# Kernel optimization log

Measured on AMD Instinct MI355X. Metric: run time of the kernel, lower is better.

Reference implementation:

```python
import jax, jax.numpy as jnp
import numpy as np
from jax import lax

STATE_LEN = 5
N_BASE = 4
C = N_BASE ** STATE_LEN          # 1024 CRF states
NZ = N_BASE + 1                  # 5 incoming transitions per state
FEAT = 320
KW = 19
STRIDE = 5
SCALE = 5.0


def _transition_idx():
    # bonito CTC_CRF.idx: predecessor state for each (state, transition) pair
    a = np.arange(C)
    idx = np.concatenate([a[:, None], np.repeat(a, N_BASE).reshape(N_BASE, -1).T], axis=1)
    return jnp.asarray(idx, dtype=jnp.int32)  # [C, NZ]


def setup_inputs() -> dict:
    key = jax.random.key(0)
    ks = jax.random.split(key, 5)
    x = jax.random.normal(ks[0], (32, 1, 4000), jnp.float32)
    conv_w = jax.random.normal(ks[1], (FEAT, 1, KW), jnp.float32) * 0.1
    conv_b = jax.random.normal(ks[2], (FEAT,), jnp.float32) * 0.1
    lin_w = jax.random.normal(ks[3], (FEAT, C * NZ), jnp.float32) * (1.0 / np.sqrt(FEAT))
    lin_b = jax.random.normal(ks[4], (C * NZ,), jnp.float32) * 0.1
    return {"x": x, "conv_w": conv_w, "conv_b": conv_b, "lin_w": lin_w, "lin_b": lin_b}


def _encoder(x, conv_w, conv_b, lin_w, lin_b):
    # x: [N, 1, L] -> strided conv -> [N, FEAT, T]
    y = lax.conv_general_dilated(x, conv_w, (STRIDE,), "SAME",
                                 dimension_numbers=("NCH", "OIH", "NCH"))
    y = jnp.tanh(y + conv_b[None, :, None])
    y = jnp.transpose(y, (2, 0, 1))  # [T, N, FEAT]
    # scaled-tanh CRF output head -> [T, N, C*NZ]
    return SCALE * jnp.tanh(jnp.einsum("tnf,fc->tnc", y, lin_w) + lin_b)


def _logZ(scores, idx):
    # log-semiring forward algorithm (alpha_0 = beta_T = 0)
    T, N, _ = scores.shape
    Ms = scores.reshape(T, N, C, NZ)
    alpha0 = jnp.zeros((N, C), scores.dtype)

    def step(alpha, Ms_t):  # Ms_t: [N, C, NZ], alpha: [N, C]
        return jax.nn.logsumexp(Ms_t + alpha[:, idx], axis=2), None

    alpha, _ = lax.scan(step, alpha0, Ms)
    return jax.nn.logsumexp(alpha, axis=1)  # [N]


def reference(x, conv_w, conv_b, lin_w, lin_b):
    idx = _transition_idx()
    scores = _encoder(x, conv_w, conv_b, lin_w, lin_b).astype(jnp.float32)  # [T, N, 5120]
    T = scores.shape[0]
    # GlobalNorm: scores - logZ / T, broadcast over time and channel dims
    return scores - _logZ(scores, idx)[:, None] / T
```

## Files before the change

kernel.cpp:

```cpp
#include <hip/hip_runtime.h>
#include <hip/hip_bf16.h>
#include <hip/hip_fp16.h>
#include <type_traits>


typedef __attribute__((ext_vector_type(8))) short bf16x8;
typedef __attribute__((ext_vector_type(4))) float f32x4;

#define T_STEPS 800
#define NBATCH 32
#define FEAT 320
#define CNZ 5120
#define MROWS (T_STEPS * NBATCH)
#define FSPLIT 480
#define BSTEPS (T_STEPS - FSPLIT)

__device__ __forceinline__ float fast_tanh(float x) {
    float e = exp2f(x * 2.8853900817779268f);
    return 1.0f - 2.0f * __builtin_amdgcn_rcpf(e + 1.0f);
}

__global__ __launch_bounds__(320) void conv_kernel(
    const float* __restrict__ x, const float* __restrict__ w,
    const float* __restrict__ b, __hip_bfloat16* __restrict__ y) {
    int m = blockIdx.x;
    int t = m >> 5, n = m & 31;
    int f = threadIdx.x;
    __shared__ float xs[19];
    int base = t * 5 - 7;
    if (f < 19) {
        int pos = base + f;
        xs[f] = (pos >= 0 && pos < 4000) ? x[n * 4000 + pos] : 0.0f;
    }
    __syncthreads();
    float acc = b[f];
#pragma unroll
    for (int k = 0; k < 19; ++k) acc = fmaf(xs[k], w[f * 19 + k], acc);
    y[(size_t)m * FEAT + f] = __float2bfloat16(fast_tanh(acc));
}

__global__ __launch_bounds__(256) void transpose_w(
    const float* __restrict__ W, __hip_bfloat16* __restrict__ Wt) {
    __shared__ float tile[64][65];
    int nb = blockIdx.x * 64, kb = blockIdx.y * 64;
    int tx = threadIdx.x & 63, ty = threadIdx.x >> 6;
#pragma unroll
    for (int r = 0; r < 64; r += 4)
        tile[ty + r][tx] = W[(size_t)(kb + ty + r) * CNZ + nb + tx];
    __syncthreads();
#pragma unroll
    for (int r = 0; r < 64; r += 4) {
        int nn = ty + r;
        Wt[(size_t)(nb + nn) * FEAT + kb + tx] = __float2bfloat16(tile[tx][nn]);
    }
}

#define GBM 128
#define GBN 128
#define GBK 64
#define LDK 72

__global__ __launch_bounds__(256) void gemm_kernel(
    const __hip_bfloat16* __restrict__ A,
    const __hip_bfloat16* __restrict__ Bt,
    const float* __restrict__ bias,
    float* __restrict__ out,
    __half* __restrict__ s16) {
    __shared__ __align__(16) short As[GBM * LDK];
    __shared__ __align__(16) short Bs[GBN * LDK];
    const int K = FEAT;
    int bm0 = blockIdx.x * GBM;
    int bn0 = blockIdx.y * GBN;
    int tid = threadIdx.x;
    int wave = tid >> 6, lane = tid & 63;
    int wm = (wave >> 1) * 64, wn = (wave & 1) * 64;
    int col = lane & 15, quad = lane >> 4;

    f32x4 acc[4][4];
#pragma unroll
    for (int i = 0; i < 4; ++i)
#pragma unroll
        for (int j = 0; j < 4; ++j) acc[i][j] = (f32x4){0.f, 0.f, 0.f, 0.f};

    for (int k0 = 0; k0 < K; k0 += GBK) {
#pragma unroll
        for (int p = 0; p < 4; ++p) {
            int i = p * 256 + tid;
            int row = i >> 3, cg = i & 7;
            *(int4*)&As[row * LDK + cg * 8] =
                *(const int4*)&A[(size_t)(bm0 + row) * K + k0 + cg * 8];
            *(int4*)&Bs[row * LDK + cg * 8] =
                *(const int4*)&Bt[(size_t)(bn0 + row) * K + k0 + cg * 8];
        }
        __syncthreads();
#pragma unroll
        for (int kk = 0; kk < GBK; kk += 32) {
            bf16x8 af[4], bfr[4];
#pragma unroll
            for (int i = 0; i < 4; ++i)
                af[i] = *(bf16x8*)&As[(wm + i * 16 + col) * LDK + kk + quad * 8];
#pragma unroll
            for (int j = 0; j < 4; ++j)
                bfr[j] = *(bf16x8*)&Bs[(wn + j * 16 + col) * LDK + kk + quad * 8];
#pragma unroll
            for (int i = 0; i < 4; ++i)
#pragma unroll
                for (int j = 0; j < 4; ++j)
                    acc[i][j] = __builtin_amdgcn_mfma_f32_16x16x32_bf16(
                        af[i], bfr[j], acc[i][j], 0, 0, 0);
        }
        __syncthreads();
    }
#pragma unroll
    for (int j = 0; j < 4; ++j) {
        int n_g = bn0 + wn + j * 16 + col;
        float bj = bias[n_g];
#pragma unroll
        for (int i = 0; i < 4; ++i) {
            int m_base = bm0 + wm + i * 16 + quad * 4;
#pragma unroll
            for (int r = 0; r < 4; ++r) {
                size_t idx = (size_t)(m_base + r) * CNZ + n_g;
                float v = 5.0f * fast_tanh(acc[i][j][r] + bj);
                out[idx] = v;
                if (s16) s16[idx] = __float2half(v);
            }
        }
    }
}


__device__ __forceinline__ float lse5_2(float s0, float s1, float s2, float s3,
                                        float s4, float a0, float a1, float a2,
                                        float a3, float a4) {
    const float L2E = 1.4426950408889634f;
    float x0 = fmaf(s0, L2E, a0);
    float x1 = fmaf(s1, L2E, a1);
    float x2 = fmaf(s2, L2E, a2);
    float x3 = fmaf(s3, L2E, a3);
    float x4 = fmaf(s4, L2E, a4);
    float mx = fmaxf(fmaxf(fmaxf(x0, x1), fmaxf(x2, x3)), x4);
    float sum = __builtin_amdgcn_exp2f(x0 - mx) + __builtin_amdgcn_exp2f(x1 - mx) +
                __builtin_amdgcn_exp2f(x2 - mx) + __builtin_amdgcn_exp2f(x3 - mx) +
                __builtin_amdgcn_exp2f(x4 - mx);
    return __builtin_amdgcn_logf(sum) + mx;
}

__device__ __forceinline__ float cvh(ushort u) { __half h = *(__half*)&u; return __half2float(h); }
__device__ __forceinline__ float cvh(float f) { return f; }

template<bool FP16>
__global__ __launch_bounds__(512) void fb_kernel(
    const void* __restrict__ sc, float* __restrict__ alphaF,
    float* __restrict__ betaB) {
    __shared__ __align__(16) float A0[1024];
    __shared__ __align__(16) float A1[1024];
    const int tid = threadIdx.x;
    const int n = blockIdx.x & 31;
    const int dir = blockIdx.x >> 5;

    *(float2*)&A0[2 * tid] = make_float2(0.f, 0.f);
    __syncthreads();

    const size_t row = (size_t)NBATCH * CNZ;

    if (dir == 0) {
        const int q = tid >> 1;
        const uint* fbu = (const uint*)((const __half*)sc + (size_t)n * CNZ) +
                          (size_t)tid * 5;
        const float2* fbf = (const float2*)((const float*)sc + (size_t)n * CNZ +
                          (size_t)tid * 10);

#define LDF(P, TT) do { int tc_ = (TT) < FSPLIT ? (TT) : (FSPLIT - 1);         \
    if constexpr (FP16) { const uint* pp_ = fbu + (size_t)tc_ * 81920;         \
        P[0] = pp_[0]; P[1] = pp_[1]; P[2] = pp_[2]; P[3] = pp_[3]; P[4] = pp_[4]; } \
    else { const float2* pp_ = fbf + (size_t)tc_ * 81920; float2* d_ = (float2*)P; \
        d_[0] = pp_[0]; d_[1] = pp_[1]; d_[2] = pp_[2]; d_[3] = pp_[3]; d_[4] = pp_[4]; } \
} while (0)

#define UNP(P, s) do { if constexpr (FP16) {                                   \
        float2 f0_ = __half22float2(*(__half2*)&P[0]);                         \
        float2 f1_ = __half22float2(*(__half2*)&P[1]);                         \
        float2 f2_ = __half22float2(*(__half2*)&P[2]);                         \
        float2 f3_ = __half22float2(*(__half2*)&P[3]);                         \
        float2 f4_ = __half22float2(*(__half2*)&P[4]);                         \
        s[0]=f0_.x; s[1]=f0_.y; s[2]=f1_.x; s[3]=f1_.y; s[4]=f2_.x;            \
        s[5]=f2_.y; s[6]=f3_.x; s[7]=f3_.y; s[8]=f4_.x; s[9]=f4_.y; }          \
    else { const float* f_ = (const float*)P;                                  \
        s[0]=f_[0]; s[1]=f_[1]; s[2]=f_[2]; s[3]=f_[3]; s[4]=f_[4];            \
        s[5]=f_[5]; s[6]=f_[6]; s[7]=f_[7]; s[8]=f_[8]; s[9]=f_[9]; }          \
} while (0)

#define FSTEP(P, TT, cur, nxt) do { float s_[10]; UNP(P, s_); LDF(P, TT);      \
    float aq0_ = (cur)[q], aq1_ = (cur)[q + 256];                              \
    float aq2_ = (cur)[q + 512], aq3_ = (cur)[q + 768];                        \
    float2 ao_ = *(const float2*)&(cur)[2 * tid];                              \
    float r0_ = lse5_2(s_[0], s_[1], s_[2], s_[3], s_[4], ao_.x, aq0_, aq1_, aq2_, aq3_); \
    float r1_ = lse5_2(s_[5], s_[6], s_[7], s_[8], s_[9], ao_.y, aq0_, aq1_, aq2_, aq3_); \
    *(float2*)&(nxt)[2 * tid] = make_float2(r0_, r1_);                         \
    __syncthreads();                                                           \
} while (0)

        uint P0[10], P1[10], P2[10], P3[10];
        LDF(P0, 0); LDF(P1, 1); LDF(P2, 2); LDF(P3, 3);
        for (int t = 0; t < FSPLIT; t += 4) {
            FSTEP(P0, t + 4, A0, A1);
            FSTEP(P1, t + 5, A1, A0);
            FSTEP(P2, t + 6, A0, A1);
            FSTEP(P3, t + 7, A1, A0);
        }
        *(float2*)&alphaF[(size_t)n * 1024 + 2 * tid] = *(const float2*)&A0[2 * tid];
    } else {
        using ET = std::conditional_t<FP16, ushort, float>;
        const int p0 = 2 * tid;
        const int g = p0 & 255;
        const int hi = p0 >> 8;
        const size_t o_self = (size_t)10 * tid;
        const size_t gb = (size_t)20 * g + 1 + hi;
        const ET* bb = (const ET*)sc + (size_t)n * CNZ;
        const int sbase = (8 * tid) & 1023;

#define LDB(E, KK) do { int kc_ = (KK) < BSTEPS ? (KK) : (BSTEPS - 1);         \
    const ET* pb_ = bb + (size_t)(T_STEPS - 1 - kc_) * row;                    \
    E[0] = pb_[o_self];      E[1] = pb_[gb];       E[2] = pb_[gb + 5];         \
    E[3] = pb_[gb + 10];     E[4] = pb_[gb + 15];  E[5] = pb_[o_self + 5];     \
    E[6] = pb_[gb + 20];     E[7] = pb_[gb + 25];  E[8] = pb_[gb + 30];        \
    E[9] = pb_[gb + 35];                                                       \
} while (0)

#define BSTEP(E, KK, cur, nxt) do { float s_[10];                              \
    s_[0]=cvh(E[0]); s_[1]=cvh(E[1]); s_[2]=cvh(E[2]); s_[3]=cvh(E[3]);        \
    s_[4]=cvh(E[4]); s_[5]=cvh(E[5]); s_[6]=cvh(E[6]); s_[7]=cvh(E[7]);        \
    s_[8]=cvh(E[8]); s_[9]=cvh(E[9]); LDB(E, KK);                              \
    float2 bs_ = *(const float2*)&(cur)[2 * tid];                              \
    float4 b0_ = *(const float4*)&(cur)[sbase];                                \
    float4 b1_ = *(const float4*)&(cur)[sbase + 4];                            \
    float r0_ = lse5_2(s_[0], s_[1], s_[2], s_[3], s_[4], bs_.x, b0_.x, b0_.y, b0_.z, b0_.w); \
    float r1_ = lse5_2(s_[5], s_[6], s_[7], s_[8], s_[9], bs_.y, b1_.x, b1_.y, b1_.z, b1_.w); \
    *(float2*)&(nxt)[2 * tid] = make_float2(r0_, r1_);                         \
    __syncthreads();                                                           \
} while (0)

        ET E0[10], E1[10], E2[10], E3[10];
        LDB(E0, 0); LDB(E1, 1); LDB(E2, 2); LDB(E3, 3);
        for (int k = 0; k < BSTEPS; k += 4) {
            BSTEP(E0, k + 4, A0, A1);
            BSTEP(E1, k + 5, A1, A0);
            BSTEP(E2, k + 6, A0, A1);
            BSTEP(E3, k + 7, A1, A0);
        }
        *(float2*)&betaB[(size_t)n * 1024 + 2 * tid] = *(const float2*)&A0[2 * tid];
    }
}

__global__ __launch_bounds__(256) void combine_kernel(
    const float* __restrict__ aF, const float* __restrict__ bB,
    float* __restrict__ corr) {
    __shared__ float R[256];
    int n = blockIdx.x, tid = threadIdx.x;
    float4 a = *(const float4*)&aF[(size_t)n * 1024 + 4 * tid];
    float4 b = *(const float4*)&bB[(size_t)n * 1024 + 4 * tid];
    float x0 = a.x + b.x, x1 = a.y + b.y, x2 = a.z + b.z, x3 = a.w + b.w;
    float m = fmaxf(fmaxf(x0, x1), fmaxf(x2, x3));
    R[tid] = m;
    __syncthreads();
#pragma unroll
    for (int s = 128; s > 0; s >>= 1) {
        if (tid < s) R[tid] = fmaxf(R[tid], R[tid + s]);
        __syncthreads();
    }
    float mx = R[0];
    __syncthreads();
    float sm = exp2f(x0 - mx) + exp2f(x1 - mx) + exp2f(x2 - mx) + exp2f(x3 - mx);
    R[tid] = sm;
    __syncthreads();
#pragma unroll
    for (int s = 128; s > 0; s >>= 1) {
        if (tid < s) R[tid] += R[tid + s];
        __syncthreads();
    }
    if (tid == 0)
        corr[n] = (log2f(R[0]) + mx) * 0.6931471805599453f * (1.0f / (float)T_STEPS);
}

__global__ __launch_bounds__(256) void sub_kernel(
    float* __restrict__ out, const float* __restrict__ corr) {
    size_t i4 = (size_t)blockIdx.x * blockDim.x + threadIdx.x;
    float cc = corr[(i4 / (CNZ / 4)) & (NBATCH - 1)];
    float4* o4 = (float4*)out;
    float4 v = o4[i4];
    v.x -= cc; v.y -= cc; v.z -= cc; v.w -= cc;
    o4[i4] = v;
}

extern "C" void kernel_launch(void* const* d_in, const int* in_sizes, int n_in,
                              void* d_out, int out_size, void* d_ws, size_t ws_size,
                              hipStream_t stream) {
    const float* x      = (const float*)d_in[0];
    const float* conv_w = (const float*)d_in[1];
    const float* conv_b = (const float*)d_in[2];
    const float* lin_w  = (const float*)d_in[3];
    const float* lin_b  = (const float*)d_in[4];
    float* out = (float*)d_out;

    const size_t Y_OFF    = 0;
    const size_t WT_OFF   = 16384000;
    const size_t CORR_OFF = 19660800;
    const size_t AF_OFF   = 19661056;
    const size_t BB_OFF   = 19792128;
    const size_t S16_OFF  = 19923200;
    const size_t NEED16   = S16_OFF + (size_t)MROWS * CNZ * 2;

    char* ws = (char*)d_ws;
    __hip_bfloat16* y  = (__hip_bfloat16*)(ws + Y_OFF);
    __hip_bfloat16* wt = (__hip_bfloat16*)(ws + WT_OFF);
    float* corr = (float*)(ws + CORR_OFF);
    float* aF   = (float*)(ws + AF_OFF);
    float* bB   = (float*)(ws + BB_OFF);
    bool fp16_path = ws_size >= NEED16;
    __half* s16 = fp16_path ? (__half*)(ws + S16_OFF) : nullptr;

    conv_kernel<<<MROWS, 320, 0, stream>>>(x, conv_w, conv_b, y);
    transpose_w<<<dim3(CNZ / 64, FEAT / 64), 256, 0, stream>>>(lin_w, wt);
    gemm_kernel<<<dim3(MROWS / GBM, CNZ / GBN), 256, 0, stream>>>(y, wt, lin_b, out, s16);
    if (fp16_path)
        fb_kernel<true><<<64, 512, 0, stream>>>(s16, aF, bB);
    else
        fb_kernel<false><<<64, 512, 0, stream>>>(out, aF, bB);
    combine_kernel<<<NBATCH, 256, 0, stream>>>(aF, bB, corr);
    sub_kernel<<<(out_size / 4) / 256, 256, 0, stream>>>(out, corr);
}
```

Baseline: 1.416 ms.

## Add transposed fp16 score copy for backward pass and rebuild output from fp16

The GEMM epilogue now also writes a second fp16 copy of the scores, laid out transposed per transition so the backward recursion can issue wide contiguous loads instead of scattered scalar gathers. Because backward steps should now cost about the same as forward steps, the forward/backward split point moves to the midpoint. When workspace allows, the GEMM skips the fp32 output write and the final subtraction kernel rebuilds the fp32 output from the fp16 scores. This cuts global memory traffic but gives outputs with only fp16 precision, and it needs twice the fp16 workspace.

```diff
diff --git a/kernel.cpp b/kernel.cpp
--- a/kernel.cpp
+++ b/kernel.cpp
@@ -1,23 +1,29 @@
 #include <hip/hip_runtime.h>
 #include <hip/hip_bf16.h>
 #include <hip/hip_fp16.h>
-#include <type_traits>
 
 
 typedef __attribute__((ext_vector_type(8))) short bf16x8;
 typedef __attribute__((ext_vector_type(4))) float f32x4;
+typedef unsigned int uint4u __attribute__((ext_vector_type(4), aligned(4)));
 
 #define T_STEPS 800
 #define NBATCH 32
 #define FEAT 320
 #define CNZ 5120
 #define MROWS (T_STEPS * NBATCH)
-#define FSPLIT 480
+#define FSPLIT 400
 #define BSTEPS (T_STEPS - FSPLIT)
+#define ROWB 327680
 
 __device__ __forceinline__ float fast_tanh(float x) {
     float e = exp2f(x * 2.8853900817779268f);
     return 1.0f - 2.0f * __builtin_amdgcn_rcpf(e + 1.0f);
+}
+
+__device__ __forceinline__ float2 h2f(uint u) {
+    __half2 h = *(__half2*)&u;
+    return __half22float2(h);
 }
 
 __global__ __launch_bounds__(320) void conv_kernel(
@@ -65,7 +71,9 @@
     const __hip_bfloat16* __restrict__ Bt,
     const float* __restrict__ bias,
     float* __restrict__ out,
-    __half* __restrict__ s16) {
+    __half* __restrict__ s16n,
+    __half* __restrict__ s16t,
+    int write_out) {
     __shared__ __align__(16) short As[GBM * LDK];
     __shared__ __align__(16) short Bs[GBN * LDK];
     const int K = FEAT;
@@ -115,15 +123,21 @@
     for (int j = 0; j < 4; ++j) {
         int n_g = bn0 + wn + j * 16 + col;
         float bj = bias[n_g];
+        uint c = (uint)n_g / 5u;
+        uint z = (uint)n_g - 5u * c;
+        size_t t_off = (size_t)z * 1024 + c;
 #pragma unroll
         for (int i = 0; i < 4; ++i) {
             int m_base = bm0 + wm + i * 16 + quad * 4;
 #pragma unroll
             for (int r = 0; r < 4; ++r) {
-                size_t idx = (size_t)(m_base + r) * CNZ + n_g;
+                int m = m_base + r;
+                size_t idx = (size_t)m * CNZ + n_g;
                 float v = 5.0f * fast_tanh(acc[i][j][r] + bj);
-                out[idx] = v;
-                if (s16) s16[idx] = __float2half(v);
+                if (write_out) out[idx] = v;
+                __half hv = __float2half(v);
+                if (s16n) s16n[idx] = hv;
+                if (s16t) s16t[(size_t)m * CNZ + t_off] = hv;
             }
         }
     }
@@ -146,13 +160,10 @@
     return __builtin_amdgcn_logf(sum) + mx;
 }
 
-__device__ __forceinline__ float cvh(ushort u) { __half h = *(__half*)&u; return __half2float(h); }
-__device__ __forceinline__ float cvh(float f) { return f; }
-
-template<bool FP16>
+template<int MODE>
 __global__ __launch_bounds__(512) void fb_kernel(
-    const void* __restrict__ sc, float* __restrict__ alphaF,
-    float* __restrict__ betaB) {
+    const void* __restrict__ nat, const void* __restrict__ tr,
+    float* __restrict__ alphaF, float* __restrict__ betaB) {
     __shared__ __align__(16) float A0[1024];
     __shared__ __align__(16) float A1[1024];
     const int tid = threadIdx.x;
@@ -162,92 +173,148 @@
     *(float2*)&A0[2 * tid] = make_float2(0.f, 0.f);
     __syncthreads();
 
-    const size_t row = (size_t)NBATCH * CNZ;
-
     if (dir == 0) {
         const int q = tid >> 1;
-        const uint* fbu = (const uint*)((const __half*)sc + (size_t)n * CNZ) +
-                          (size_t)tid * 5;
-        const float2* fbf = (const float2*)((const float*)sc + (size_t)n * CNZ +
-                          (size_t)tid * 10);
-
-#define LDF(P, TT) do { int tc_ = (TT) < FSPLIT ? (TT) : (FSPLIT - 1);         \
-    if constexpr (FP16) { const uint* pp_ = fbu + (size_t)tc_ * 81920;         \
-        P[0] = pp_[0]; P[1] = pp_[1]; P[2] = pp_[2]; P[3] = pp_[3]; P[4] = pp_[4]; } \
-    else { const float2* pp_ = fbf + (size_t)tc_ * 81920; float2* d_ = (float2*)P; \
-        d_[0] = pp_[0]; d_[1] = pp_[1]; d_[2] = pp_[2]; d_[3] = pp_[3]; d_[4] = pp_[4]; } \
-} while (0)
-
-#define UNP(P, s) do { if constexpr (FP16) {                                   \
-        float2 f0_ = __half22float2(*(__half2*)&P[0]);                         \
-        float2 f1_ = __half22float2(*(__half2*)&P[1]);                         \
-        float2 f2_ = __half22float2(*(__half2*)&P[2]);                         \
-        float2 f3_ = __half22float2(*(__half2*)&P[3]);                         \
-        float2 f4_ = __half22float2(*(__half2*)&P[4]);                         \
-        s[0]=f0_.x; s[1]=f0_.y; s[2]=f1_.x; s[3]=f1_.y; s[4]=f2_.x;            \
-        s[5]=f2_.y; s[6]=f3_.x; s[7]=f3_.y; s[8]=f4_.x; s[9]=f4_.y; }          \
-    else { const float* f_ = (const float*)P;                                  \
-        s[0]=f_[0]; s[1]=f_[1]; s[2]=f_[2]; s[3]=f_[3]; s[4]=f_[4];            \
-        s[5]=f_[5]; s[6]=f_[6]; s[7]=f_[7]; s[8]=f_[8]; s[9]=f_[9]; }          \
-} while (0)
-
-#define FSTEP(P, TT, cur, nxt) do { float s_[10]; UNP(P, s_); LDF(P, TT);      \
+
+        if constexpr (MODE == 2) {
+            const char* fbn = (const char*)nat +
+                              ((size_t)n * CNZ + (size_t)tid * 10) * 2;
+
+#define LDF2(V, S, TT) do { int tc_ = (TT) < FSPLIT ? (TT) : (FSPLIT - 1);     \
+    const char* p_ = fbn + (size_t)tc_ * ROWB;                                 \
+    V = *(const uint4u*)p_; S = *(const uint*)(p_ + 16);                       \
+} while (0)
+
+#define FSTEP2(V, S, TT, cur, nxt) do {                                        \
+    float2 f0_ = h2f(V.x), f1_ = h2f(V.y), f2_ = h2f(V.z), f3_ = h2f(V.w);     \
+    float2 f4_ = h2f(S);                                                       \
+    LDF2(V, S, TT);                                                            \
     float aq0_ = (cur)[q], aq1_ = (cur)[q + 256];                              \
     float aq2_ = (cur)[q + 512], aq3_ = (cur)[q + 768];                        \
     float2 ao_ = *(const float2*)&(cur)[2 * tid];                              \
-    float r0_ = lse5_2(s_[0], s_[1], s_[2], s_[3], s_[4], ao_.x, aq0_, aq1_, aq2_, aq3_); \
-    float r1_ = lse5_2(s_[5], s_[6], s_[7], s_[8], s_[9], ao_.y, aq0_, aq1_, aq2_, aq3_); \
+    float r0_ = lse5_2(f0_.x, f0_.y, f1_.x, f1_.y, f2_.x, ao_.x, aq0_, aq1_, aq2_, aq3_); \
+    float r1_ = lse5_2(f2_.y, f3_.x, f3_.y, f4_.x, f4_.y, ao_.y, aq0_, aq1_, aq2_, aq3_); \
     *(float2*)&(nxt)[2 * tid] = make_float2(r0_, r1_);                         \
     __syncthreads();                                                           \
 } while (0)
 
-        uint P0[10], P1[10], P2[10], P3[10];
-        LDF(P0, 0); LDF(P1, 1); LDF(P2, 2); LDF(P3, 3);
-        for (int t = 0; t < FSPLIT; t += 4) {
-            FSTEP(P0, t + 4, A0, A1);
-            FSTEP(P1, t + 5, A1, A0);
-            FSTEP(P2, t + 6, A0, A1);
-            FSTEP(P3, t + 7, A1, A0);
+            uint4u P0v, P1v, P2v, P3v;
+            uint P0s, P1s, P2s, P3s;
+            LDF2(P0v, P0s, 0); LDF2(P1v, P1s, 1);
+            LDF2(P2v, P2s, 2); LDF2(P3v, P3s, 3);
+            for (int t = 0; t < FSPLIT; t += 4) {
+                FSTEP2(P0v, P0s, t + 4, A0, A1);
+                FSTEP2(P1v, P1s, t + 5, A1, A0);
+                FSTEP2(P2v, P2s, t + 6, A0, A1);
+                FSTEP2(P3v, P3s, t + 7, A1, A0);
+            }
+        } else {
+            const float2* fbf = (const float2*)((const float*)nat +
+                                (size_t)n * CNZ + (size_t)tid * 10);
+
+#define LDF1(Q, TT) do { int tc_ = (TT) < FSPLIT ? (TT) : (FSPLIT - 1);        \
+    const float2* p_ = fbf + (size_t)tc_ * 81920;                              \
+    Q[0] = p_[0]; Q[1] = p_[1]; Q[2] = p_[2]; Q[3] = p_[3]; Q[4] = p_[4];      \
+} while (0)
+
+#define FSTEP1(Q, TT, cur, nxt) do {                                           \
+    float s0_ = Q[0].x, s1_ = Q[0].y, s2_ = Q[1].x, s3_ = Q[1].y, s4_ = Q[2].x;\
+    float u0_ = Q[2].y, u1_ = Q[3].x, u2_ = Q[3].y, u3_ = Q[4].x, u4_ = Q[4].y;\
+    LDF1(Q, TT);                                                               \
+    float aq0_ = (cur)[q], aq1_ = (cur)[q + 256];                              \
+    float aq2_ = (cur)[q + 512], aq3_ = (cur)[q + 768];                        \
+    float2 ao_ = *(const float2*)&(cur)[2 * tid];                              \
+    float r0_ = lse5_2(s0_, s1_, s2_, s3_, s4_, ao_.x, aq0_, aq1_, aq2_, aq3_);\
+    float r1_ = lse5_2(u0_, u1_, u2_, u3_, u4_, ao_.y, aq0_, aq1_, aq2_, aq3_);\
+    *(float2*)&(nxt)[2 * tid] = make_float2(r0_, r1_);                         \
+    __syncthreads();                                                           \
+} while (0)
+
+            float2 Q0[5], Q1[5], Q2[5], Q3[5];
+            LDF1(Q0, 0); LDF1(Q1, 1); LDF1(Q2, 2); LDF1(Q3, 3);
+            for (int t = 0; t < FSPLIT; t += 4) {
+                FSTEP1(Q0, t + 4, A0, A1);
+                FSTEP1(Q1, t + 5, A1, A0);
+                FSTEP1(Q2, t + 6, A0, A1);
+                FSTEP1(Q3, t + 7, A1, A0);
+            }
         }
         *(float2*)&alphaF[(size_t)n * 1024 + 2 * tid] = *(const float2*)&A0[2 * tid];
     } else {
-        using ET = std::conditional_t<FP16, ushort, float>;
         const int p0 = 2 * tid;
         const int g = p0 & 255;
         const int hi = p0 >> 8;
-        const size_t o_self = (size_t)10 * tid;
-        const size_t gb = (size_t)20 * g + 1 + hi;
-        const ET* bb = (const ET*)sc + (size_t)n * CNZ;
         const int sbase = (8 * tid) & 1023;
 
-#define LDB(E, KK) do { int kc_ = (KK) < BSTEPS ? (KK) : (BSTEPS - 1);         \
-    const ET* pb_ = bb + (size_t)(T_STEPS - 1 - kc_) * row;                    \
+        if constexpr (MODE >= 1) {
+            const char* btg = (const char*)tr +
+                ((size_t)n * CNZ + (size_t)(1 + hi) * 1024 + (size_t)(4 * g)) * 2;
+            const char* bts = (const char*)tr +
+                ((size_t)n * CNZ + (size_t)p0) * 2;
+
+#define LDB2(V, S, KK) do { int kc_ = (KK) < BSTEPS ? (KK) : (BSTEPS - 1);     \
+    size_t o_ = (size_t)(T_STEPS - 1 - kc_) * ROWB;                            \
+    V = *(const uint4u*)(btg + o_); S = *(const uint*)(bts + o_);              \
+} while (0)
+
+#define BSTEP2(V, S, KK, cur, nxt) do {                                        \
+    float2 g0_ = h2f(V.x), g1_ = h2f(V.y), g2_ = h2f(V.z), g3_ = h2f(V.w);     \
+    float2 sf_ = h2f(S);                                                       \
+    LDB2(V, S, KK);                                                            \
+    float2 bs_ = *(const float2*)&(cur)[2 * tid];                              \
+    float4 b0_ = *(const float4*)&(cur)[sbase];                                \
+    float4 b1_ = *(const float4*)&(cur)[sbase + 4];                            \
+    float r0_ = lse5_2(sf_.x, g0_.x, g0_.y, g1_.x, g1_.y, bs_.x, b0_.x, b0_.y, b0_.z, b0_.w); \
+    float r1_ = lse5_2(sf_.y, g2_.x, g2_.y, g3_.x, g3_.y, bs_.y, b1_.x, b1_.y, b1_.z, b1_.w); \
+    *(float2*)&(nxt)[2 * tid] = make_float2(r0_, r1_);                         \
+    __syncthreads();                                                           \
+} while (0)
+
+            uint4u E0v, E1v, E2v, E3v;
+            uint E0s, E1s, E2s, E3s;
+            LDB2(E0v, E0s, 0); LDB2(E1v, E1s, 1);
+            LDB2(E2v, E2s, 2); LDB2(E3v, E3s, 3);
+            for (int k = 0; k < BSTEPS; k += 4) {
+                BSTEP2(E0v, E0s, k + 4, A0, A1);
+                BSTEP2(E1v, E1s, k + 5, A1, A0);
+                BSTEP2(E2v, E2s, k + 6, A0, A1);
+                BSTEP2(E3v, E3s, k + 7, A1, A0);
+            }
+        } else {
+            const size_t o_self = (size_t)10 * tid;
+            const size_t gb = (size_t)20 * g + 1 + hi;
+            const float* bb = (const float*)nat + (size_t)n * CNZ;
+            const size_t row = (size_t)NBATCH * CNZ;
+
+#define LDB1(E, KK) do { int kc_ = (KK) < BSTEPS ? (KK) : (BSTEPS - 1);        \
+    const float* pb_ = bb + (size_t)(T_STEPS - 1 - kc_) * row;                 \
     E[0] = pb_[o_self];      E[1] = pb_[gb];       E[2] = pb_[gb + 5];         \
     E[3] = pb_[gb + 10];     E[4] = pb_[gb + 15];  E[5] = pb_[o_self + 5];     \
     E[6] = pb_[gb + 20];     E[7] = pb_[gb + 25];  E[8] = pb_[gb + 30];        \
     E[9] = pb_[gb + 35];                                                       \
 } while (0)
 
-#define BSTEP(E, KK, cur, nxt) do { float s_[10];                              \
-    s_[0]=cvh(E[0]); s_[1]=cvh(E[1]); s_[2]=cvh(E[2]); s_[3]=cvh(E[3]);        \
-    s_[4]=cvh(E[4]); s_[5]=cvh(E[5]); s_[6]=cvh(E[6]); s_[7]=cvh(E[7]);        \
-    s_[8]=cvh(E[8]); s_[9]=cvh(E[9]); LDB(E, KK);                              \
+#define BSTEP1(E, KK, cur, nxt) do {                                           \
+    float s0_=E[0], s1_=E[1], s2_=E[2], s3_=E[3], s4_=E[4];                    \
+    float u0_=E[5], u1_=E[6], u2_=E[7], u3_=E[8], u4_=E[9];                    \
+    LDB1(E, KK);                                                               \
     float2 bs_ = *(const float2*)&(cur)[2 * tid];                              \
     float4 b0_ = *(const float4*)&(cur)[sbase];                                \
     float4 b1_ = *(const float4*)&(cur)[sbase + 4];                            \
-    float r0_ = lse5_2(s_[0], s_[1], s_[2], s_[3], s_[4], bs_.x, b0_.x, b0_.y, b0_.z, b0_.w); \
-    float r1_ = lse5_2(s_[5], s_[6], s_[7], s_[8], s_[9], bs_.y, b1_.x, b1_.y, b1_.z, b1_.w); \
+    float r0_ = lse5_2(s0_, s1_, s2_, s3_, s4_, bs_.x, b0_.x, b0_.y, b0_.z, b0_.w); \
+    float r1_ = lse5_2(u0_, u1_, u2_, u3_, u4_, bs_.y, b1_.x, b1_.y, b1_.z, b1_.w); \
     *(float2*)&(nxt)[2 * tid] = make_float2(r0_, r1_);                         \
     __syncthreads();                                                           \
 } while (0)
 
-        ET E0[10], E1[10], E2[10], E3[10];
-        LDB(E0, 0); LDB(E1, 1); LDB(E2, 2); LDB(E3, 3);
-        for (int k = 0; k < BSTEPS; k += 4) {
-            BSTEP(E0, k + 4, A0, A1);
-            BSTEP(E1, k + 5, A1, A0);
-            BSTEP(E2, k + 6, A0, A1);
-            BSTEP(E3, k + 7, A1, A0);
+            float E0[10], E1[10], E2[10], E3[10];
+            LDB1(E0, 0); LDB1(E1, 1); LDB1(E2, 2); LDB1(E3, 3);
+            for (int k = 0; k < BSTEPS; k += 4) {
+                BSTEP1(E0, k + 4, A0, A1);
+                BSTEP1(E1, k + 5, A1, A0);
+                BSTEP1(E2, k + 6, A0, A1);
+                BSTEP1(E3, k + 7, A1, A0);
+            }
         }
         *(float2*)&betaB[(size_t)n * 1024 + 2 * tid] = *(const float2*)&A0[2 * tid];
     }
@@ -293,6 +360,19 @@
     o4[i4] = v;
 }
 
+__global__ __launch_bounds__(256) void sub_mat_kernel(
+    const __half* __restrict__ s16, const float* __restrict__ corr,
+    float* __restrict__ out) {
+    size_t i = (size_t)blockIdx.x * blockDim.x + threadIdx.x;
+    float cc = corr[(i / (CNZ / 8)) & (NBATCH - 1)];
+    uint4 h = ((const uint4*)s16)[i];
+    float2 f0 = h2f(h.x), f1 = h2f(h.y), f2 = h2f(h.z), f3 = h2f(h.w);
+    float4 o0 = make_float4(f0.x - cc, f0.y - cc, f1.x - cc, f1.y - cc);
+    float4 o1 = make_float4(f2.x - cc, f2.y - cc, f3.x - cc, f3.y - cc);
+    ((float4*)out)[2 * i] = o0;
+    ((float4*)out)[2 * i + 1] = o1;
+}
+
 extern "C" void kernel_launch(void* const* d_in, const int* in_sizes, int n_in,
                               void* d_out, int out_size, void* d_ws, size_t ws_size,
                               hipStream_t stream) {
@@ -308,8 +388,10 @@
     const size_t CORR_OFF = 19660800;
     const size_t AF_OFF   = 19661056;
     const size_t BB_OFF   = 19792128;
-    const size_t S16_OFF  = 19923200;
-    const size_t NEED16   = S16_OFF + (size_t)MROWS * CNZ * 2;
+    const size_t P0_OFF   = 19923200;
+    const size_t SC_BYTES = (size_t)MROWS * CNZ * 2;
+    const size_t NEED_A   = P0_OFF + 2 * SC_BYTES;
+    const size_t NEED_B   = P0_OFF + SC_BYTES;
 
     char* ws = (char*)d_ws;
     __hip_bfloat16* y  = (__hip_bfloat16*)(ws + Y_OFF);
@@ -317,16 +399,35 @@
     float* corr = (float*)(ws + CORR_OFF);
     float* aF   = (float*)(ws + AF_OFF);
     float* bB   = (float*)(ws + BB_OFF);
-    bool fp16_path = ws_size >= NEED16;
-    __half* s16 = fp16_path ? (__half*)(ws + S16_OFF) : nullptr;
+
+    __half* s16n = nullptr;
+    __half* s16t = nullptr;
+    int mode = 0;
+    if (ws_size >= NEED_A) {
+        s16n = (__half*)(ws + P0_OFF);
+        s16t = (__half*)(ws + P0_OFF + SC_BYTES);
+        mode = 2;
+    } else if (ws_size >= NEED_B) {
+        s16t = (__half*)(ws + P0_OFF);
+        mode = 1;
+    }
 
     conv_kernel<<<MROWS, 320, 0, stream>>>(x, conv_w, conv_b, y);
     transpose_w<<<dim3(CNZ / 64, FEAT / 64), 256, 0, stream>>>(lin_w, wt);
-    gemm_kernel<<<dim3(MROWS / GBM, CNZ / GBN), 256, 0, stream>>>(y, wt, lin_b, out, s16);
-    if (fp16_path)
-        fb_kernel<true><<<64, 512, 0, stream>>>(s16, aF, bB);
+    gemm_kernel<<<dim3(MROWS / GBM, CNZ / GBN), 256, 0, stream>>>(
+        y, wt, lin_b, out, s16n, s16t, mode != 2 ? 1 : 0);
+
+    if (mode == 2)
+        fb_kernel<2><<<64, 512, 0, stream>>>(s16n, s16t, aF, bB);
+    else if (mode == 1)
+        fb_kernel<1><<<64, 512, 0, stream>>>(out, s16t, aF, bB);
     else
-        fb_kernel<false><<<64, 512, 0, stream>>>(out, aF, bB);
+        fb_kernel<0><<<64, 512, 0, stream>>>(out, nullptr, aF, bB);
+
     combine_kernel<<<NBATCH, 256, 0, stream>>>(aF, bB, corr);
-    sub_kernel<<<(out_size / 4) / 256, 256, 0, stream>>>(out, corr);
-}
+
+    if (mode == 2)
+        sub_mat_kernel<<<(out_size / 8) / 256, 256, 0, stream>>>(s16n, corr, out);
+    else
+        sub_kernel<<<(out_size / 4) / 256, 256, 0, stream>>>(out, corr);
+}
```

Result: faster. 1.314 ms (-7.2%).
